# Optimization experiments

Hardware: AMD Instinct MI355X
Metric: run time of the kernel (lower is better)

The kernel has to match this reference:

```python
import jax, jax.numpy as jnp
import numpy as np

EPS = 1e-06


def setup_inputs() -> dict:
    key = jax.random.key(0)
    k1, k2 = jax.random.split(key)
    B, T, N, D, L = 8, 4096, 9, 512, 32
    sources = jax.random.normal(k1, (B, T, N, D), dtype=jnp.float32)
    queries = jax.random.normal(k2, (L, D), dtype=jnp.float32)
    layer_idx = 5
    return {"sources": sources, "queries": queries, "layer_idx": layer_idx}


def reference(sources, queries, layer_idx):
    # sources: (B, T, N, d) stacked block representations (v_stack)
    # RMSNorm keys (no learnable scale)
    rms = jnp.sqrt(jnp.mean(sources * sources, axis=-1, keepdims=True) + EPS)
    k_stack = sources / rms                      # (B, T, N, d)
    w = queries[layer_idx]                       # (d,)
    scores = jnp.einsum('btnd,d->btn', k_stack, w)   # (B, T, N)
    alpha = jax.nn.softmax(scores, axis=-1)          # (B, T, N)
    h = jnp.einsum('btn,btnd->btd', alpha, sources)  # (B, T, d)
    return h
```

## Files before the change

### kernel.cpp

```cpp
#include <hip/hip_runtime.h>
#include <stdint.h>
#include <stddef.h>

static constexpr int D = 512;
static constexpr int N = 9;
static constexpr float EPS = 1e-6f;

__global__ __launch_bounds__(256) void block_attn(
    const float4* __restrict__ src4,
    const float4* __restrict__ q4,
    const int*   __restrict__ layer_idx,
    float4* __restrict__ out4,
    int bt_total)
{
    const int lane = threadIdx.x & 63;
    const int wave = threadIdx.x >> 6;
    const int bt   = blockIdx.x * 4 + wave;
    if (bt >= bt_total) return;

    const int li = layer_idx[0];
    const float4* qp = q4 + (size_t)li * (D / 4);
    const float4 w0 = qp[lane];
    const float4 w1 = qp[64 + lane];

    const float4* p = src4 + (size_t)bt * (size_t)(N * (D / 4)) + lane;

    float4 s0[N], s1[N];
    float  ss[N], dt[N];

#pragma unroll
    for (int n = 0; n < N; ++n) {
        const float4 a = p[n * (D / 4)];
        const float4 b = p[n * (D / 4) + 64];
        s0[n] = a; s1[n] = b;

        float s2 = a.x * a.x;
        s2 = fmaf(a.y, a.y, s2); s2 = fmaf(a.z, a.z, s2); s2 = fmaf(a.w, a.w, s2);
        s2 = fmaf(b.x, b.x, s2); s2 = fmaf(b.y, b.y, s2);
        s2 = fmaf(b.z, b.z, s2); s2 = fmaf(b.w, b.w, s2);

        float dd = a.x * w0.x;
        dd = fmaf(a.y, w0.y, dd); dd = fmaf(a.z, w0.z, dd); dd = fmaf(a.w, w0.w, dd);
        dd = fmaf(b.x, w1.x, dd); dd = fmaf(b.y, w1.y, dd);
        dd = fmaf(b.z, w1.z, dd); dd = fmaf(b.w, w1.w, dd);

        ss[n] = s2; dt[n] = dd;
    }

#pragma unroll
    for (int m = 1; m < 64; m <<= 1) {
#pragma unroll
        for (int n = 0; n < N; ++n) {
            ss[n] += __shfl_xor(ss[n], m, 64);
            dt[n] += __shfl_xor(dt[n], m, 64);
        }
    }

    float score[N];
#pragma unroll
    for (int n = 0; n < N; ++n)
        score[n] = dt[n] * rsqrtf(ss[n] * (1.0f / 512.0f) + EPS);

    float mx = score[0];
#pragma unroll
    for (int n = 1; n < N; ++n) mx = fmaxf(mx, score[n]);
    float asum = 0.f;
    float alpha[N];
#pragma unroll
    for (int n = 0; n < N; ++n) { alpha[n] = __expf(score[n] - mx); asum += alpha[n]; }
    const float inv = 1.0f / asum;

    float4 h0 = {0.f, 0.f, 0.f, 0.f};
    float4 h1 = {0.f, 0.f, 0.f, 0.f};
#pragma unroll
    for (int n = 0; n < N; ++n) {
        const float an = alpha[n] * inv;
        h0.x = fmaf(an, s0[n].x, h0.x); h0.y = fmaf(an, s0[n].y, h0.y);
        h0.z = fmaf(an, s0[n].z, h0.z); h0.w = fmaf(an, s0[n].w, h0.w);
        h1.x = fmaf(an, s1[n].x, h1.x); h1.y = fmaf(an, s1[n].y, h1.y);
        h1.z = fmaf(an, s1[n].z, h1.z); h1.w = fmaf(an, s1[n].w, h1.w);
    }

    float4* op = out4 + (size_t)bt * (D / 4);
    op[lane]      = h0;
    op[64 + lane] = h1;
}

extern "C" void kernel_launch(void* const* d_in, const int* in_sizes, int n_in,
                              void* d_out, int out_size, void* d_ws, size_t ws_size,
                              hipStream_t stream) {
    (void)n_in; (void)d_ws; (void)ws_size;
    const float4* src = (const float4*)d_in[0];
    const float4* q   = (const float4*)d_in[1];
    const int*    li  = (const int*)d_in[2];
    float4* out = (float4*)d_out;

    const bool elem_units = (in_sizes[2] == 1);
    const long long src_elems = elem_units ? (long long)in_sizes[0]
                                           : (long long)in_sizes[0] / 4;
    const long long bt_total = src_elems / (long long)(N * D);

    const int blocks = (int)((bt_total + 3) / 4);
    block_attn<<<blocks, 256, 0, stream>>>(src, q, li, out, (int)bt_total);
}
```

Measured before the change: 764.5 us.

## Split each (b,t) row across a full 256-thread block with LDS reduction

```diff
diff --git a/kernel.cpp b/kernel.cpp
--- a/kernel.cpp
+++ b/kernel.cpp
@@ -6,45 +6,34 @@
 static constexpr int N = 9;
 static constexpr float EPS = 1e-6f;
 
-__global__ __launch_bounds__(256) void block_attn(
-    const float4* __restrict__ src4,
-    const float4* __restrict__ q4,
+__global__ __launch_bounds__(256, 8) void block_attn(
+    const float2* __restrict__ src2,
+    const float2* __restrict__ q2,
     const int*   __restrict__ layer_idx,
-    float4* __restrict__ out4,
+    float2* __restrict__ out2,
     int bt_total)
 {
-    const int lane = threadIdx.x & 63;
-    const int wave = threadIdx.x >> 6;
-    const int bt   = blockIdx.x * 4 + wave;
+    const int tid  = threadIdx.x;
+    const int lane = tid & 63;
+    const int wave = tid >> 6;
+    const int bt   = blockIdx.x;
     if (bt >= bt_total) return;
 
+    __shared__ __align__(16) float red[2 * N][4];
+
     const int li = layer_idx[0];
-    const float4* qp = q4 + (size_t)li * (D / 4);
-    const float4 w0 = qp[lane];
-    const float4 w1 = qp[64 + lane];
+    const float2 w = q2[(size_t)li * (D / 2) + tid];
 
-    const float4* p = src4 + (size_t)bt * (size_t)(N * (D / 4)) + lane;
+    const float2* p = src2 + (size_t)bt * (size_t)(N * (D / 2)) + tid;
 
-    float4 s0[N], s1[N];
+    float2 s[N];
     float  ss[N], dt[N];
-
 #pragma unroll
     for (int n = 0; n < N; ++n) {
-        const float4 a = p[n * (D / 4)];
-        const float4 b = p[n * (D / 4) + 64];
-        s0[n] = a; s1[n] = b;
-
-        float s2 = a.x * a.x;
-        s2 = fmaf(a.y, a.y, s2); s2 = fmaf(a.z, a.z, s2); s2 = fmaf(a.w, a.w, s2);
-        s2 = fmaf(b.x, b.x, s2); s2 = fmaf(b.y, b.y, s2);
-        s2 = fmaf(b.z, b.z, s2); s2 = fmaf(b.w, b.w, s2);
-
-        float dd = a.x * w0.x;
-        dd = fmaf(a.y, w0.y, dd); dd = fmaf(a.z, w0.z, dd); dd = fmaf(a.w, w0.w, dd);
-        dd = fmaf(b.x, w1.x, dd); dd = fmaf(b.y, w1.y, dd);
-        dd = fmaf(b.z, w1.z, dd); dd = fmaf(b.w, w1.w, dd);
-
-        ss[n] = s2; dt[n] = dd;
+        const float2 v = p[n * (D / 2)];
+        s[n] = v;
+        ss[n] = fmaf(v.x, v.x, v.y * v.y);
+        dt[n] = fmaf(v.x, w.x, v.y * w.y);
     }
 
 #pragma unroll
@@ -56,10 +45,20 @@
         }
     }
 
+    if (lane < 2 * N) {
+        red[lane][wave] = (lane < N) ? ss[lane] : dt[lane - N];
+    }
+    __syncthreads();
+
     float score[N];
 #pragma unroll
-    for (int n = 0; n < N; ++n)
-        score[n] = dt[n] * rsqrtf(ss[n] * (1.0f / 512.0f) + EPS);
+    for (int n = 0; n < N; ++n) {
+        const float4 a = *(const float4*)red[n];
+        const float4 b = *(const float4*)red[n + N];
+        const float S = (a.x + a.y) + (a.z + a.w);
+        const float T = (b.x + b.y) + (b.z + b.w);
+        score[n] = T * rsqrtf(S * (1.0f / 512.0f) + EPS);
+    }
 
     float mx = score[0];
 #pragma unroll
@@ -70,36 +69,30 @@
     for (int n = 0; n < N; ++n) { alpha[n] = __expf(score[n] - mx); asum += alpha[n]; }
     const float inv = 1.0f / asum;
 
-    float4 h0 = {0.f, 0.f, 0.f, 0.f};
-    float4 h1 = {0.f, 0.f, 0.f, 0.f};
+    float2 h = {0.f, 0.f};
 #pragma unroll
     for (int n = 0; n < N; ++n) {
         const float an = alpha[n] * inv;
-        h0.x = fmaf(an, s0[n].x, h0.x); h0.y = fmaf(an, s0[n].y, h0.y);
-        h0.z = fmaf(an, s0[n].z, h0.z); h0.w = fmaf(an, s0[n].w, h0.w);
-        h1.x = fmaf(an, s1[n].x, h1.x); h1.y = fmaf(an, s1[n].y, h1.y);
-        h1.z = fmaf(an, s1[n].z, h1.z); h1.w = fmaf(an, s1[n].w, h1.w);
+        h.x = fmaf(an, s[n].x, h.x);
+        h.y = fmaf(an, s[n].y, h.y);
     }
 
-    float4* op = out4 + (size_t)bt * (D / 4);
-    op[lane]      = h0;
-    op[64 + lane] = h1;
+    out2[(size_t)bt * (D / 2) + tid] = h;
 }
 
 extern "C" void kernel_launch(void* const* d_in, const int* in_sizes, int n_in,
                               void* d_out, int out_size, void* d_ws, size_t ws_size,
                               hipStream_t stream) {
     (void)n_in; (void)d_ws; (void)ws_size;
-    const float4* src = (const float4*)d_in[0];
-    const float4* q   = (const float4*)d_in[1];
+    const float2* src = (const float2*)d_in[0];
+    const float2* q   = (const float2*)d_in[1];
     const int*    li  = (const int*)d_in[2];
-    float4* out = (float4*)d_out;
+    float2* out = (float2*)d_out;
 
     const bool elem_units = (in_sizes[2] == 1);
     const long long src_elems = elem_units ? (long long)in_sizes[0]
                                            : (long long)in_sizes[0] / 4;
     const long long bt_total = src_elems / (long long)(N * D);
 
-    const int blocks = (int)((bt_total + 3) / 4);
-    block_attn<<<blocks, 256, 0, stream>>>(src, q, li, out, (int)bt_total);
+    block_attn<<<(int)bt_total, 256, 0, stream>>>(src, q, li, out, (int)bt_total);
 }
```

Result: slower. 822.3 us (+7.6%).
